# Optimization experiments

Measured on AMD Instinct MI355X. Metric: run time of the kernel, lower is better.

## Reference

```python
import jax, jax.numpy as jnp
import numpy as np

B, L, C, H, W = 4, 4096, 1024, 16, 512
D = C // H            # head_dim = 64
STRIDE = W // 2


def setup_inputs() -> dict:
    key = jax.random.key(0)
    k0, k1, k2 = jax.random.split(key, 3)
    s = 0.02
    return {
        "x": jax.random.normal(k0, (B, L, C), jnp.float32),
        "w_qkv": jax.random.normal(k1, (C, 3 * C), jnp.float32) * s,
        "b_qkv": jnp.zeros((3 * C,), jnp.float32),
        "w_out": jax.random.normal(k2, (C, C), jnp.float32) * s,
        "b_out": jnp.zeros((C,), jnp.float32),
    }


def _local_attention(x, w_qkv, b_qkv, w_out, b_out):
    b, l, c = x.shape
    pad = (-l) % W  # pad seq to multiple of window_size (0 here)
    x = jnp.pad(x, ((0, 0), (0, pad), (0, 0)))
    lp = l + pad
    qkv = (x @ w_qkv + b_qkv).reshape(b, lp, 3, H, D).transpose(2, 0, 3, 1, 4)
    q, k, v = qkv[0], qkv[1], qkv[2]  # each [B, H, Lp, D]
    nw = (lp - W) // STRIDE + 1       # number of overlapping windows
    # window token indices [nw, W]
    idx = jnp.arange(nw)[:, None] * STRIDE + jnp.arange(W)[None, :]
    qw = q[:, :, idx, :]  # [B, H, nw, W, D]
    kw = k[:, :, idx, :]
    vw = v[:, :, idx, :]
    # non-causal (bidirectional=True) attention within each window,
    # flash-attn default softmax scale = head_dim**-0.5
    scores = jnp.einsum('bhnqd,bhnkd->bhnqk', qw, kw) / jnp.sqrt(jnp.float32(D))
    probs = jax.nn.softmax(scores, axis=-1)
    ow = jnp.einsum('bhnqk,bhnkd->bhnqd', probs, vw)  # [B, H, nw, W, D]
    # concatenate window outputs along sequence, back to [B, nw*W, C]
    o = ow.transpose(0, 2, 3, 1, 4).reshape(b, nw * W, c)
    o = o @ w_out + b_out
    return o[:, :l, :]


def reference(x, w_qkv, b_qkv, w_out, b_out):
    return _local_attention(x, w_qkv, b_qkv, w_out, b_out)
```

## Files before the change

kernel.cpp:

```cpp
#include <hip/hip_runtime.h>

#define LQ 2304

typedef __attribute__((ext_vector_type(8))) short bf16x8;
typedef __attribute__((ext_vector_type(8))) unsigned short u16x8;
typedef __attribute__((ext_vector_type(4))) float f32x4;
typedef __attribute__((ext_vector_type(4))) unsigned int u32x4;

#define MFMA(a, b, c) __builtin_amdgcn_mfma_f32_16x16x32_bf16((a), (b), (c), 0, 0, 0)
#define AS1 __attribute__((address_space(1)))
#define AS3 __attribute__((address_space(3)))

static __device__ __forceinline__ unsigned short f2bf(float f) {
  unsigned int u = __builtin_bit_cast(unsigned int, f);
  u += 0x7fffu + ((u >> 16) & 1u);
  return (unsigned short)(u >> 16);
}

static __device__ __forceinline__ unsigned int pkbf(float hi, float lo) {
  return __builtin_amdgcn_perm(__builtin_bit_cast(unsigned int, hi),
                               __builtin_bit_cast(unsigned int, lo), 0x07060302u);
}

static __device__ __forceinline__ void lds16(const unsigned short* g, unsigned short* l) {
  __builtin_amdgcn_global_load_lds((AS1 const unsigned int*)g, (AS3 unsigned int*)l, 16, 0, 0);
}

__global__ __launch_bounds__(256) void conv_x(const float* __restrict__ x,
                                              unsigned short* __restrict__ xbf) {
  int b = blockIdx.y;
  int g = blockIdx.x * 256 + threadIdx.x;
  int row = g >> 7, c8 = (g & 127) * 8;
  const float* src = x + ((size_t)b * 4096 + row) * 1024 + c8;
  float4 f0 = *(const float4*)src;
  float4 f1 = *(const float4*)(src + 4);
  u16x8 u;
  u[0] = f2bf(f0.x); u[1] = f2bf(f0.y); u[2] = f2bf(f0.z); u[3] = f2bf(f0.w);
  u[4] = f2bf(f1.x); u[5] = f2bf(f1.y); u[6] = f2bf(f1.z); u[7] = f2bf(f1.w);
  *(u16x8*)(xbf + ((size_t)b * 2304 + row) * 1024 + c8) = u;
}

__global__ __launch_bounds__(256) void transpose_conv(const float* __restrict__ src,
                                                      unsigned short* __restrict__ dst,
                                                      int K, int N) {
  __shared__ float t[32][33];
  int bn = blockIdx.x * 32, bk = blockIdx.y * 32;
  int tx = threadIdx.x, ty = threadIdx.y;
  for (int i = ty; i < 32; i += 8)
    t[i][tx] = src[(size_t)(bk + i) * N + bn + tx];
  __syncthreads();
  for (int i = ty; i < 32; i += 8)
    dst[(size_t)(bn + i) * K + bk + tx] = f2bf(t[tx][i]);
}

#define K2SCALE 0.18033688011112042f
__global__ __launch_bounds__(256) void qkv_gemm(const unsigned short* __restrict__ xbf,
                                                const float* __restrict__ bqkv,
                                                const unsigned short* __restrict__ wT,
                                                unsigned short* __restrict__ qws,
                                                unsigned short* __restrict__ kws,
                                                unsigned short* __restrict__ vws) {
  __shared__ __align__(16) unsigned short As[128 * 32];
  __shared__ __align__(16) unsigned short Bs[128 * 32];
  const int tid = threadIdx.x;
  const int mt = blockIdx.y;
  const int nt = blockIdx.x;
  const int bidx = mt / 18;
  const int l0 = (mt % 18) * 128;
  const int n0 = nt * 128;
  const int lane = tid & 63, wv = tid >> 6;
  const int wm = (wv >> 1) * 64, wn = (wv & 1) * 64;
  const int l16 = lane & 15, quad = lane >> 4;

  const unsigned short* ga = xbf + ((size_t)bidx * LQ + l0 + wv * 32 + (lane >> 2)) * 1024 + (lane & 3) * 8;
  const unsigned short* gb = wT + (size_t)(n0 + wv * 32 + (lane >> 2)) * 1024 + (lane & 3) * 8;
  unsigned short* la = As + wv * 1024;
  unsigned short* lb = Bs + wv * 1024;

  const f32x4 zero4 = {0.f, 0.f, 0.f, 0.f};
  f32x4 acc[4][4];
#pragma unroll
  for (int i = 0; i < 4; i++)
#pragma unroll
    for (int j = 0; j < 4; j++) acc[i][j] = zero4;

  for (int k0 = 0; k0 < 1024; k0 += 32) {
    __syncthreads();
    lds16(ga, la);
    lds16(ga + 16 * 1024, la + 512);
    lds16(gb, lb);
    lds16(gb + 16 * 1024, lb + 512);
    __syncthreads();
    bf16x8 af[4], bfv[4];
#pragma unroll
    for (int i = 0; i < 4; i++)
      af[i] = *(const bf16x8*)(&As[(wm + i * 16 + l16) * 32 + quad * 8]);
#pragma unroll
    for (int j = 0; j < 4; j++)
      bfv[j] = *(const bf16x8*)(&Bs[(wn + j * 16 + l16) * 32 + quad * 8]);
#pragma unroll
    for (int i = 0; i < 4; i++)
#pragma unroll
      for (int j = 0; j < 4; j++)
        acc[i][j] = MFMA(af[i], bfv[j], acc[i][j]);
    ga += 32;
    gb += 32;
  }

#pragma unroll
  for (int j = 0; j < 4; j++) {
    int col = n0 + wn + j * 16 + l16;
    int which = col >> 10;
    int hcol = (col >> 6) & 15;
    int dcol = col & 63;
    unsigned short* dst = which == 0 ? qws : (which == 1 ? kws : vws);
    float scale = which == 0 ? K2SCALE : 1.0f;
    float bias = bqkv[col];
    size_t cbase = ((size_t)bidx * 16 + hcol) * LQ * 64 + dcol;
#pragma unroll
    for (int i = 0; i < 4; i++) {
      int lrow = l0 + wm + i * 16 + quad * 4;
#pragma unroll
      for (int r = 0; r < 4; r++)
        dst[cbase + (size_t)(lrow + r) * 64] = f2bf((acc[i][j][r] + bias) * scale);
    }
  }
}

#define KSTR 72
#define VSTR 520
#define ATTN_LDS ((512 * KSTR + 64 * VSTR) * 2)

__global__ __launch_bounds__(512, 2) void attn_kernel(const unsigned short* __restrict__ q,
                                                      const unsigned short* __restrict__ k,
                                                      const unsigned short* __restrict__ v,
                                                      unsigned short* __restrict__ o) {
  extern __shared__ unsigned short lds[];
  unsigned short* Ks = lds;
  unsigned short* Vt = lds + 512 * KSTR;
  const int n = blockIdx.x, h = blockIdx.y, b = blockIdx.z;
  const size_t base = (((size_t)b * 16 + h) * LQ + n * 256) * 64;
  const unsigned short* qg = q + base;
  const unsigned short* kg = k + base;
  const unsigned short* vg = v + base;
  const int tid = threadIdx.x;
  const int lane = tid & 63, wv = tid >> 6;

  for (int i = tid; i < 4096; i += 512) {
    int key = i >> 3, part = i & 7;
    *(u16x8*)(&Ks[key * KSTR + part * 8]) = *(const u16x8*)(kg + (size_t)key * 64 + part * 8);
  }
  for (int it = 0; it < 8; it++) {
    int key = it * 64 + lane;
    u16x8 raw = *(const u16x8*)(vg + (size_t)key * 64 + wv * 8);
    int pos = (key & ~31) + ((key >> 2) & 3) * 8 + ((key >> 4) & 1) * 4 + (key & 3);
#pragma unroll
    for (int t = 0; t < 8; t++) Vt[(wv * 8 + t) * VSTR + pos] = raw[t];
  }
  __syncthreads();

  const int l16 = lane & 15, quad = lane >> 4;
  const f32x4 zero4 = {0.f, 0.f, 0.f, 0.f};
  const float RB = 0.002815015607053277f;

  bf16x8 qf0[4], qf1[4];
#pragma unroll
  for (int qs = 0; qs < 4; qs++) {
    int qrow = wv * 64 + qs * 16 + l16;
    qf0[qs] = *(const bf16x8*)(qg + (size_t)qrow * 64 + quad * 8);
    qf1[qs] = *(const bf16x8*)(qg + (size_t)qrow * 64 + quad * 8 + 32);
  }
  f32x4 O[4][4];
#pragma unroll
  for (int qs = 0; qs < 4; qs++)
#pragma unroll
    for (int dt = 0; dt < 4; dt++) O[qs][dt] = zero4;
  float lsum[4] = {0.f, 0.f, 0.f, 0.f};

  for (int c = 0; c < 16; c++) {
    const unsigned short* kr0 = &Ks[(c * 32 + l16) * KSTR + quad * 8];
    bf16x8 ka0 = *(const bf16x8*)kr0;
    bf16x8 ka1 = *(const bf16x8*)(kr0 + 32);
    bf16x8 kb0 = *(const bf16x8*)(kr0 + 16 * KSTR);
    bf16x8 kb1 = *(const bf16x8*)(kr0 + 16 * KSTR + 32);
    bf16x8 vf[4];
#pragma unroll
    for (int dt = 0; dt < 4; dt++)
      vf[dt] = *(const bf16x8*)(&Vt[(dt * 16 + l16) * VSTR + c * 32 + quad * 8]);
#pragma unroll
    for (int qs = 0; qs < 4; qs++) {
      f32x4 s0 = zero4, s1 = zero4;
      s0 = MFMA(ka0, qf0[qs], s0);
      s0 = MFMA(ka1, qf1[qs], s0);
      s1 = MFMA(kb0, qf0[qs], s1);
      s1 = MFMA(kb1, qf1[qs], s1);
      float p0[4], p1[4], ls = 0.f;
#pragma unroll
      for (int r = 0; r < 4; r++) {
        p0[r] = __builtin_amdgcn_exp2f(s0[r] + RB);
        p1[r] = __builtin_amdgcn_exp2f(s1[r] + RB);
        ls += p0[r] + p1[r];
      }
      lsum[qs] += ls;
      u32x4 pw;
      pw[0] = pkbf(p0[1], p0[0]);
      pw[1] = pkbf(p0[3], p0[2]);
      pw[2] = pkbf(p1[1], p1[0]);
      pw[3] = pkbf(p1[3], p1[2]);
      bf16x8 pf = __builtin_bit_cast(bf16x8, pw);
#pragma unroll
      for (int dt = 0; dt < 4; dt++)
        O[qs][dt] = MFMA(pf, vf[dt], O[qs][dt]);
    }
  }

#pragma unroll
  for (int qs = 0; qs < 4; qs++) {
    float ls = lsum[qs];
    ls += __shfl_xor(ls, 16);
    ls += __shfl_xor(ls, 32);
    float linv = 1.0f / ls;
    float li[4];
#pragma unroll
    for (int r = 0; r < 4; r++) li[r] = __shfl(linv, quad * 4 + r);
    size_t orow = (size_t)b * 4096 + n * 512 + wv * 64 + qs * 16;
#pragma unroll
    for (int dt = 0; dt < 4; dt++) {
      int col = h * 64 + dt * 16 + l16;
#pragma unroll
      for (int r = 0; r < 4; r++)
        o[(orow + quad * 4 + r) * 1024 + col] = f2bf(O[qs][dt][r] * li[r]);
    }
  }
}

__global__ __launch_bounds__(256) void out_gemm(const unsigned short* __restrict__ A,
                                                const unsigned short* __restrict__ wT,
                                                const float* __restrict__ bout,
                                                float* __restrict__ out) {
  __shared__ __align__(16) unsigned short As[128 * 32];
  __shared__ __align__(16) unsigned short Bs[128 * 32];
  const int tid = threadIdx.x;
  const int m0 = blockIdx.y * 128;
  const int n0 = blockIdx.x * 128;
  const int lane = tid & 63, wv = tid >> 6;
  const int wm = (wv >> 1) * 64, wn = (wv & 1) * 64;
  const int l16 = lane & 15, quad = lane >> 4;

  const unsigned short* ga = A + (size_t)(m0 + wv * 32 + (lane >> 2)) * 1024 + (lane & 3) * 8;
  const unsigned short* gb = wT + (size_t)(n0 + wv * 32 + (lane >> 2)) * 1024 + (lane & 3) * 8;
  unsigned short* la = As + wv * 1024;
  unsigned short* lb = Bs + wv * 1024;

  const f32x4 zero4 = {0.f, 0.f, 0.f, 0.f};
  f32x4 acc[4][4];
#pragma unroll
  for (int i = 0; i < 4; i++)
#pragma unroll
    for (int j = 0; j < 4; j++) acc[i][j] = zero4;

  for (int k0 = 0; k0 < 1024; k0 += 32) {
    __syncthreads();
    lds16(ga, la);
    lds16(ga + 16 * 1024, la + 512);
    lds16(gb, lb);
    lds16(gb + 16 * 1024, lb + 512);
    __syncthreads();
    bf16x8 af[4], bfv[4];
#pragma unroll
    for (int i = 0; i < 4; i++)
      af[i] = *(const bf16x8*)(&As[(wm + i * 16 + l16) * 32 + quad * 8]);
#pragma unroll
    for (int j = 0; j < 4; j++)
      bfv[j] = *(const bf16x8*)(&Bs[(wn + j * 16 + l16) * 32 + quad * 8]);
#pragma unroll
    for (int i = 0; i < 4; i++)
#pragma unroll
      for (int j = 0; j < 4; j++)
        acc[i][j] = MFMA(af[i], bfv[j], acc[i][j]);
    ga += 32;
    gb += 32;
  }

#pragma unroll
  for (int j = 0; j < 4; j++) {
    int col = n0 + wn + j * 16 + l16;
    float bias = bout[col];
#pragma unroll
    for (int i = 0; i < 4; i++) {
      int row = m0 + wm + i * 16 + quad * 4;
#pragma unroll
      for (int r = 0; r < 4; r++)
        out[(size_t)(row + r) * 1024 + col] = acc[i][j][r] + bias;
    }
  }
}

#define WQKVT_OFF 0u
#define WOUTT_OFF (WQKVT_OFF + 3072u * 1024u * 2u)
#define QWS_OFF   (WOUTT_OFF + 1024u * 1024u * 2u)
#define KVQ_SZ    (4u * 16u * 2304u * 64u * 2u)
#define KWS_OFF   (QWS_OFF + KVQ_SZ)
#define VWS_OFF   (KWS_OFF + KVQ_SZ)
#define OWS_OFF   (VWS_OFF + KVQ_SZ)
#define XBF_OFF   OWS_OFF

extern "C" void kernel_launch(void* const* d_in, const int* in_sizes, int n_in,
                              void* d_out, int out_size, void* d_ws, size_t ws_size,
                              hipStream_t stream) {
  const float* x     = (const float*)d_in[0];
  const float* w_qkv = (const float*)d_in[1];
  const float* b_qkv = (const float*)d_in[2];
  const float* w_out = (const float*)d_in[3];
  const float* b_out = (const float*)d_in[4];
  float* out = (float*)d_out;
  char* ws = (char*)d_ws;

  unsigned short* wqkvT = (unsigned short*)(ws + WQKVT_OFF);
  unsigned short* woutT = (unsigned short*)(ws + WOUTT_OFF);
  unsigned short* qws   = (unsigned short*)(ws + QWS_OFF);
  unsigned short* kws   = (unsigned short*)(ws + KWS_OFF);
  unsigned short* vws   = (unsigned short*)(ws + VWS_OFF);
  unsigned short* ows   = (unsigned short*)(ws + OWS_OFF);
  unsigned short* xbf   = (unsigned short*)(ws + XBF_OFF);

  conv_x<<<dim3(1152, 4), 256, 0, stream>>>(x, xbf);
  transpose_conv<<<dim3(96, 32), dim3(32, 8), 0, stream>>>(w_qkv, wqkvT, 1024, 3072);
  transpose_conv<<<dim3(32, 32), dim3(32, 8), 0, stream>>>(w_out, woutT, 1024, 1024);

  qkv_gemm<<<dim3(24, 72), 256, 0, stream>>>(xbf, b_qkv, wqkvT, qws, kws, vws);

  (void)hipFuncSetAttribute((const void*)attn_kernel,
                            hipFuncAttributeMaxDynamicSharedMemorySize, ATTN_LDS);
  attn_kernel<<<dim3(8, 16, 4), 512, ATTN_LDS, stream>>>(qws, kws, vws, ows);

  out_gemm<<<dim3(8, 128), 256, 0, stream>>>(ows, woutT, b_out, out);
}
```

Before: 330.2 us.

## Fuse preprocessing kernels, deepen GEMM K-tile with XOR swizzle, tile attention K/V

The three conversion and transpose launches become one preprocess kernel that dispatches on block index, which saves two launches. Both GEMMs now stage 64-wide K tiles with an XOR-swizzled LDS layout, which halves the barrier count per K and aims to reduce bank conflicts. The attention kernel now loads K and V in 128-key chunks into a smaller static LDS buffer instead of staging the full 512-key window up front. That cuts LDS use and may raise occupancy, at the cost of extra barriers per chunk.

Result: no change. 325.7 us (-1.3%).

```diff
diff --git a/kernel.cpp b/kernel.cpp
--- a/kernel.cpp
+++ b/kernel.cpp
@@ -26,31 +26,46 @@
   __builtin_amdgcn_global_load_lds((AS1 const unsigned int*)g, (AS3 unsigned int*)l, 16, 0, 0);
 }
 
-__global__ __launch_bounds__(256) void conv_x(const float* __restrict__ x,
-                                              unsigned short* __restrict__ xbf) {
-  int b = blockIdx.y;
-  int g = blockIdx.x * 256 + threadIdx.x;
-  int row = g >> 7, c8 = (g & 127) * 8;
-  const float* src = x + ((size_t)b * 4096 + row) * 1024 + c8;
-  float4 f0 = *(const float4*)src;
-  float4 f1 = *(const float4*)(src + 4);
-  u16x8 u;
-  u[0] = f2bf(f0.x); u[1] = f2bf(f0.y); u[2] = f2bf(f0.z); u[3] = f2bf(f0.w);
-  u[4] = f2bf(f1.x); u[5] = f2bf(f1.y); u[6] = f2bf(f1.z); u[7] = f2bf(f1.w);
-  *(u16x8*)(xbf + ((size_t)b * 2304 + row) * 1024 + c8) = u;
-}
-
-__global__ __launch_bounds__(256) void transpose_conv(const float* __restrict__ src,
+static __device__ __forceinline__ void transpose_body(const float* __restrict__ src,
                                                       unsigned short* __restrict__ dst,
-                                                      int K, int N) {
-  __shared__ float t[32][33];
-  int bn = blockIdx.x * 32, bk = blockIdx.y * 32;
-  int tx = threadIdx.x, ty = threadIdx.y;
+                                                      int K, int N, int bx, int by, int tid,
+                                                      float (*t)[33]) {
+  int bn = bx * 32, bk = by * 32;
+  int tx = tid & 31, ty = tid >> 5;
   for (int i = ty; i < 32; i += 8)
     t[i][tx] = src[(size_t)(bk + i) * N + bn + tx];
   __syncthreads();
   for (int i = ty; i < 32; i += 8)
     dst[(size_t)(bn + i) * K + bk + tx] = f2bf(t[tx][i]);
+}
+
+__global__ __launch_bounds__(256) void preprocess(const float* __restrict__ x,
+                                                  unsigned short* __restrict__ xbf,
+                                                  const float* __restrict__ wqkv,
+                                                  unsigned short* __restrict__ wqkvT,
+                                                  const float* __restrict__ wout,
+                                                  unsigned short* __restrict__ woutT) {
+  __shared__ float t[32][33];
+  int bid = blockIdx.x, tid = threadIdx.x;
+  if (bid < 4608) {
+    int idx = bid * 256 + tid;
+    int b = idx / 294912;
+    int g = idx - b * 294912;
+    int row = g >> 7, c8 = (g & 127) * 8;
+    const float* src = x + ((size_t)b * 4096 + row) * 1024 + c8;
+    float4 f0 = *(const float4*)src;
+    float4 f1 = *(const float4*)(src + 4);
+    u16x8 u;
+    u[0] = f2bf(f0.x); u[1] = f2bf(f0.y); u[2] = f2bf(f0.z); u[3] = f2bf(f0.w);
+    u[4] = f2bf(f1.x); u[5] = f2bf(f1.y); u[6] = f2bf(f1.z); u[7] = f2bf(f1.w);
+    *(u16x8*)(xbf + ((size_t)b * 2304 + row) * 1024 + c8) = u;
+  } else if (bid < 7680) {
+    int tb = bid - 4608;
+    transpose_body(wqkv, wqkvT, 1024, 3072, tb % 96, tb / 96, tid, t);
+  } else {
+    int tb = bid - 7680;
+    transpose_body(wout, woutT, 1024, 1024, tb & 31, tb >> 5, tid, t);
+  }
 }
 
 #define K2SCALE 0.18033688011112042f
@@ -60,8 +75,8 @@
                                                 unsigned short* __restrict__ qws,
                                                 unsigned short* __restrict__ kws,
                                                 unsigned short* __restrict__ vws) {
-  __shared__ __align__(16) unsigned short As[128 * 32];
-  __shared__ __align__(16) unsigned short Bs[128 * 32];
+  __shared__ __align__(16) unsigned short As[128 * 64];
+  __shared__ __align__(16) unsigned short Bs[128 * 64];
   const int tid = threadIdx.x;
   const int mt = blockIdx.y;
   const int nt = blockIdx.x;
@@ -72,10 +87,13 @@
   const int wm = (wv >> 1) * 64, wn = (wv & 1) * 64;
   const int l16 = lane & 15, quad = lane >> 4;
 
-  const unsigned short* ga = xbf + ((size_t)bidx * LQ + l0 + wv * 32 + (lane >> 2)) * 1024 + (lane & 3) * 8;
-  const unsigned short* gb = wT + (size_t)(n0 + wv * 32 + (lane >> 2)) * 1024 + (lane & 3) * 8;
-  unsigned short* la = As + wv * 1024;
-  unsigned short* lb = Bs + wv * 1024;
+  const int srow = lane >> 3;
+  const int sc = ((lane & 7) ^ srow) * 8;
+  const unsigned short* ga = xbf + ((size_t)(bidx * LQ + l0 + wv * 32 + srow)) * 1024 + sc;
+  const unsigned short* gb = wT + ((size_t)(n0 + wv * 32 + srow)) * 1024 + sc;
+  unsigned short* la = As + wv * 2048;
+  unsigned short* lb = Bs + wv * 2048;
+  const int xsw = (l16 & 7) * 8;
 
   const f32x4 zero4 = {0.f, 0.f, 0.f, 0.f};
   f32x4 acc[4][4];
@@ -84,27 +102,31 @@
 #pragma unroll
     for (int j = 0; j < 4; j++) acc[i][j] = zero4;
 
-  for (int k0 = 0; k0 < 1024; k0 += 32) {
-    __syncthreads();
-    lds16(ga, la);
-    lds16(ga + 16 * 1024, la + 512);
-    lds16(gb, lb);
-    lds16(gb + 16 * 1024, lb + 512);
-    __syncthreads();
-    bf16x8 af[4], bfv[4];
-#pragma unroll
-    for (int i = 0; i < 4; i++)
-      af[i] = *(const bf16x8*)(&As[(wm + i * 16 + l16) * 32 + quad * 8]);
-#pragma unroll
-    for (int j = 0; j < 4; j++)
-      bfv[j] = *(const bf16x8*)(&Bs[(wn + j * 16 + l16) * 32 + quad * 8]);
-#pragma unroll
-    for (int i = 0; i < 4; i++)
+  for (int k0 = 0; k0 < 1024; k0 += 64) {
+    __syncthreads();
+#pragma unroll
+    for (int j = 0; j < 4; j++) {
+      lds16(ga + j * 8 * 1024, la + j * 512);
+      lds16(gb + j * 8 * 1024, lb + j * 512);
+    }
+    __syncthreads();
+#pragma unroll
+    for (int h = 0; h < 2; h++) {
+      bf16x8 af[4], bfv[4];
+#pragma unroll
+      for (int i = 0; i < 4; i++)
+        af[i] = *(const bf16x8*)(&As[(wm + i * 16 + l16) * 64 + (((h << 5) + quad * 8) ^ xsw)]);
 #pragma unroll
       for (int j = 0; j < 4; j++)
-        acc[i][j] = MFMA(af[i], bfv[j], acc[i][j]);
-    ga += 32;
-    gb += 32;
+        bfv[j] = *(const bf16x8*)(&Bs[(wn + j * 16 + l16) * 64 + (((h << 5) + quad * 8) ^ xsw)]);
+#pragma unroll
+      for (int i = 0; i < 4; i++)
+#pragma unroll
+        for (int j = 0; j < 4; j++)
+          acc[i][j] = MFMA(af[i], bfv[j], acc[i][j]);
+    }
+    ga += 64;
+    gb += 64;
   }
 
 #pragma unroll
@@ -128,16 +150,14 @@
 }
 
 #define KSTR 72
-#define VSTR 520
-#define ATTN_LDS ((512 * KSTR + 64 * VSTR) * 2)
+#define VSTRT 136
 
 __global__ __launch_bounds__(512, 2) void attn_kernel(const unsigned short* __restrict__ q,
                                                       const unsigned short* __restrict__ k,
                                                       const unsigned short* __restrict__ v,
                                                       unsigned short* __restrict__ o) {
-  extern __shared__ unsigned short lds[];
-  unsigned short* Ks = lds;
-  unsigned short* Vt = lds + 512 * KSTR;
+  __shared__ __align__(16) unsigned short Ks[128 * KSTR];
+  __shared__ __align__(16) unsigned short Vt[64 * VSTRT];
   const int n = blockIdx.x, h = blockIdx.y, b = blockIdx.z;
   const size_t base = (((size_t)b * 16 + h) * LQ + n * 256) * 64;
   const unsigned short* qg = q + base;
@@ -145,20 +165,6 @@
   const unsigned short* vg = v + base;
   const int tid = threadIdx.x;
   const int lane = tid & 63, wv = tid >> 6;
-
-  for (int i = tid; i < 4096; i += 512) {
-    int key = i >> 3, part = i & 7;
-    *(u16x8*)(&Ks[key * KSTR + part * 8]) = *(const u16x8*)(kg + (size_t)key * 64 + part * 8);
-  }
-  for (int it = 0; it < 8; it++) {
-    int key = it * 64 + lane;
-    u16x8 raw = *(const u16x8*)(vg + (size_t)key * 64 + wv * 8);
-    int pos = (key & ~31) + ((key >> 2) & 3) * 8 + ((key >> 4) & 1) * 4 + (key & 3);
-#pragma unroll
-    for (int t = 0; t < 8; t++) Vt[(wv * 8 + t) * VSTR + pos] = raw[t];
-  }
-  __syncthreads();
-
   const int l16 = lane & 15, quad = lane >> 4;
   const f32x4 zero4 = {0.f, 0.f, 0.f, 0.f};
   const float RB = 0.002815015607053277f;
@@ -177,40 +183,60 @@
     for (int dt = 0; dt < 4; dt++) O[qs][dt] = zero4;
   float lsum[4] = {0.f, 0.f, 0.f, 0.f};
 
-  for (int c = 0; c < 16; c++) {
-    const unsigned short* kr0 = &Ks[(c * 32 + l16) * KSTR + quad * 8];
-    bf16x8 ka0 = *(const bf16x8*)kr0;
-    bf16x8 ka1 = *(const bf16x8*)(kr0 + 32);
-    bf16x8 kb0 = *(const bf16x8*)(kr0 + 16 * KSTR);
-    bf16x8 kb1 = *(const bf16x8*)(kr0 + 16 * KSTR + 32);
-    bf16x8 vf[4];
-#pragma unroll
-    for (int dt = 0; dt < 4; dt++)
-      vf[dt] = *(const bf16x8*)(&Vt[(dt * 16 + l16) * VSTR + c * 32 + quad * 8]);
-#pragma unroll
-    for (int qs = 0; qs < 4; qs++) {
-      f32x4 s0 = zero4, s1 = zero4;
-      s0 = MFMA(ka0, qf0[qs], s0);
-      s0 = MFMA(ka1, qf1[qs], s0);
-      s1 = MFMA(kb0, qf0[qs], s1);
-      s1 = MFMA(kb1, qf1[qs], s1);
-      float p0[4], p1[4], ls = 0.f;
-#pragma unroll
-      for (int r = 0; r < 4; r++) {
-        p0[r] = __builtin_amdgcn_exp2f(s0[r] + RB);
-        p1[r] = __builtin_amdgcn_exp2f(s1[r] + RB);
-        ls += p0[r] + p1[r];
+  for (int kt = 0; kt < 4; kt++) {
+    __syncthreads();
+#pragma unroll
+    for (int it = 0; it < 2; it++) {
+      int i = it * 512 + tid;
+      int key = i >> 3, part = i & 7;
+      *(u16x8*)(&Ks[key * KSTR + part * 8]) =
+          *(const u16x8*)(kg + (size_t)(kt * 128 + key) * 64 + part * 8);
+    }
+#pragma unroll
+    for (int it = 0; it < 2; it++) {
+      int key = it * 64 + lane;
+      u16x8 raw = *(const u16x8*)(vg + (size_t)(kt * 128 + key) * 64 + wv * 8);
+      int pos = (key & ~31) + ((key >> 2) & 3) * 8 + ((key >> 4) & 1) * 4 + (key & 3);
+#pragma unroll
+      for (int t = 0; t < 8; t++) Vt[(wv * 8 + t) * VSTRT + pos] = raw[t];
+    }
+    __syncthreads();
+
+    for (int c = 0; c < 4; c++) {
+      const unsigned short* kr0 = &Ks[(c * 32 + l16) * KSTR + quad * 8];
+      bf16x8 ka0 = *(const bf16x8*)kr0;
+      bf16x8 ka1 = *(const bf16x8*)(kr0 + 32);
+      bf16x8 kb0 = *(const bf16x8*)(kr0 + 16 * KSTR);
+      bf16x8 kb1 = *(const bf16x8*)(kr0 + 16 * KSTR + 32);
+      bf16x8 vf[4];
+#pragma unroll
+      for (int dt = 0; dt < 4; dt++)
+        vf[dt] = *(const bf16x8*)(&Vt[(dt * 16 + l16) * VSTRT + c * 32 + quad * 8]);
+#pragma unroll
+      for (int qs = 0; qs < 4; qs++) {
+        f32x4 s0 = zero4, s1 = zero4;
+        s0 = MFMA(ka0, qf0[qs], s0);
+        s0 = MFMA(ka1, qf1[qs], s0);
+        s1 = MFMA(kb0, qf0[qs], s1);
+        s1 = MFMA(kb1, qf1[qs], s1);
+        float p0[4], p1[4], ls = 0.f;
+#pragma unroll
+        for (int r = 0; r < 4; r++) {
+          p0[r] = __builtin_amdgcn_exp2f(s0[r] + RB);
+          p1[r] = __builtin_amdgcn_exp2f(s1[r] + RB);
+          ls += p0[r] + p1[r];
+        }
+        lsum[qs] += ls;
+        u32x4 pw;
+        pw[0] = pkbf(p0[1], p0[0]);
+        pw[1] = pkbf(p0[3], p0[2]);
+        pw[2] = pkbf(p1[1], p1[0]);
+        pw[3] = pkbf(p1[3], p1[2]);
+        bf16x8 pf = __builtin_bit_cast(bf16x8, pw);
+#pragma unroll
+        for (int dt = 0; dt < 4; dt++)
+          O[qs][dt] = MFMA(pf, vf[dt], O[qs][dt]);
       }
-      lsum[qs] += ls;
-      u32x4 pw;
-      pw[0] = pkbf(p0[1], p0[0]);
-      pw[1] = pkbf(p0[3], p0[2]);
-      pw[2] = pkbf(p1[1], p1[0]);
-      pw[3] = pkbf(p1[3], p1[2]);
-      bf16x8 pf = __builtin_bit_cast(bf16x8, pw);
-#pragma unroll
-      for (int dt = 0; dt < 4; dt++)
-        O[qs][dt] = MFMA(pf, vf[dt], O[qs][dt]);
     }
   }
 
@@ -238,8 +264,8 @@
                                                 const unsigned short* __restrict__ wT,
                                                 const float* __restrict__ bout,
                                                 float* __restrict__ out) {
-  __shared__ __align__(16) unsigned short As[128 * 32];
-  __shared__ __align__(16) unsigned short Bs[128 * 32];
+  __shared__ __align__(16) unsigned short As[128 * 64];
+  __shared__ __align__(16) unsigned short Bs[128 * 64];
   const int tid = threadIdx.x;
   const int m0 = blockIdx.y * 128;
   const int n0 = blockIdx.x * 128;
@@ -247,10 +273,13 @@
   const int wm = (wv >> 1) * 64, wn = (wv & 1) * 64;
   const int l16 = lane & 15, quad = lane >> 4;
 
-  const unsigned short* ga = A + (size_t)(m0 + wv * 32 + (lane >> 2)) * 1024 + (lane & 3) * 8;
-  const unsigned short* gb = wT + (size_t)(n0 + wv * 32 + (lane >> 2)) * 1024 + (lane & 3) * 8;
-  unsigned short* la = As + wv * 1024;
-  unsigned short* lb = Bs + wv * 1024;
+  const int srow = lane >> 3;
+  const int sc = ((lane & 7) ^ srow) * 8;
+  const unsigned short* ga = A + ((size_t)(m0 + wv * 32 + srow)) * 1024 + sc;
+  const unsigned short* gb = wT + ((size_t)(n0 + wv * 32 + srow)) * 1024 + sc;
+  unsigned short* la = As + wv * 2048;
+  unsigned short* lb = Bs + wv * 2048;
+  const int xsw = (l16 & 7) * 8;
 
   const f32x4 zero4 = {0.f, 0.f, 0.f, 0.f};
   f32x4 acc[4][4];
@@ -259,27 +288,31 @@
 #pragma unroll
     for (int j = 0; j < 4; j++) acc[i][j] = zero4;
 
-  for (int k0 = 0; k0 < 1024; k0 += 32) {
-    __syncthreads();
-    lds16(ga, la);
-    lds16(ga + 16 * 1024, la + 512);
-    lds16(gb, lb);
-    lds16(gb + 16 * 1024, lb + 512);
-    __syncthreads();
-    bf16x8 af[4], bfv[4];
-#pragma unroll
-    for (int i = 0; i < 4; i++)
-      af[i] = *(const bf16x8*)(&As[(wm + i * 16 + l16) * 32 + quad * 8]);
-#pragma unroll
-    for (int j = 0; j < 4; j++)
-      bfv[j] = *(const bf16x8*)(&Bs[(wn + j * 16 + l16) * 32 + quad * 8]);
-#pragma unroll
-    for (int i = 0; i < 4; i++)
+  for (int k0 = 0; k0 < 1024; k0 += 64) {
+    __syncthreads();
+#pragma unroll
+    for (int j = 0; j < 4; j++) {
+      lds16(ga + j * 8 * 1024, la + j * 512);
+      lds16(gb + j * 8 * 1024, lb + j * 512);
+    }
+    __syncthreads();
+#pragma unroll
+    for (int h = 0; h < 2; h++) {
+      bf16x8 af[4], bfv[4];
+#pragma unroll
+      for (int i = 0; i < 4; i++)
+        af[i] = *(const bf16x8*)(&As[(wm + i * 16 + l16) * 64 + (((h << 5) + quad * 8) ^ xsw)]);
 #pragma unroll
       for (int j = 0; j < 4; j++)
-        acc[i][j] = MFMA(af[i], bfv[j], acc[i][j]);
-    ga += 32;
-    gb += 32;
+        bfv[j] = *(const bf16x8*)(&Bs[(wn + j * 16 + l16) * 64 + (((h << 5) + quad * 8) ^ xsw)]);
+#pragma unroll
+      for (int i = 0; i < 4; i++)
+#pragma unroll
+        for (int j = 0; j < 4; j++)
+          acc[i][j] = MFMA(af[i], bfv[j], acc[i][j]);
+    }
+    ga += 64;
+    gb += 64;
   }
 
 #pragma unroll
@@ -324,15 +357,11 @@
   unsigned short* ows   = (unsigned short*)(ws + OWS_OFF);
   unsigned short* xbf   = (unsigned short*)(ws + XBF_OFF);
 
-  conv_x<<<dim3(1152, 4), 256, 0, stream>>>(x, xbf);
-  transpose_conv<<<dim3(96, 32), dim3(32, 8), 0, stream>>>(w_qkv, wqkvT, 1024, 3072);
-  transpose_conv<<<dim3(32, 32), dim3(32, 8), 0, stream>>>(w_out, woutT, 1024, 1024);
+  preprocess<<<8704, 256, 0, stream>>>(x, xbf, w_qkv, wqkvT, w_out, woutT);
 
   qkv_gemm<<<dim3(24, 72), 256, 0, stream>>>(xbf, b_qkv, wqkvT, qws, kws, vws);
 
-  (void)hipFuncSetAttribute((const void*)attn_kernel,
-                            hipFuncAttributeMaxDynamicSharedMemorySize, ATTN_LDS);
-  attn_kernel<<<dim3(8, 16, 4), 512, ATTN_LDS, stream>>>(qws, kws, vws, ows);
+  attn_kernel<<<dim3(8, 16, 4), 512, 0, stream>>>(qws, kws, vws, ows);
 
   out_gemm<<<dim3(8, 128), 256, 0, stream>>>(ows, woutT, b_out, out);
 }
```
